# Kernel tuning notes

Measured on AMD Instinct MI355X. Metric: run time of the kernel, lower is better.

Reference implementation:

```python
import jax, jax.numpy as jnp
import numpy as np

DIM = 1024
H = 16
HD = DIM // H  # 64
BASE = 10000.0


def _rope_tables(seq_len, d):
    # freqs over half-dim, then TILED (repeat) along last axis as in the torch code
    freqs = 1.0 / (BASE ** (jnp.arange(0, d, 2, dtype=jnp.float32) / d))  # [d/2]
    t = jnp.arange(seq_len, dtype=jnp.float32)
    f = jnp.outer(t, freqs)  # [S, d/2]
    cos = jnp.concatenate([jnp.cos(f), jnp.cos(f)], axis=-1)  # [S, d] (tiled, NOT interleaved)
    sin = jnp.concatenate([jnp.sin(f), jnp.sin(f)], axis=-1)
    return cos, sin


def _apply_rope(x):
    # x: [B, H, S, d]; rotation pairs adjacent elements (2i, 2i+1)
    S, d = x.shape[-2], x.shape[-1]
    cos, sin = _rope_tables(S, d)  # [S, d]
    xh = x.reshape(*x.shape[:-1], d // 2, 2)
    x_rot = jnp.stack([-xh[..., 1], xh[..., 0]], axis=-1).reshape(x.shape)
    return x * cos + x_rot * sin


def setup_inputs() -> dict:
    key = jax.random.key(0)
    ks = jax.random.split(key, 7)
    B, Sq, Sk = 16, 512, 512
    s = 0.02
    return {
        "x": jax.random.normal(ks[0], (B, Sq, DIM), jnp.float32),
        "context": jax.random.normal(ks[1], (B, Sk, DIM), jnp.float32),
        "Wq": jax.random.normal(ks[2], (DIM, DIM), jnp.float32) * s,
        "Wk": jax.random.normal(ks[3], (DIM, DIM), jnp.float32) * s,
        "Wv": jax.random.normal(ks[4], (DIM, DIM), jnp.float32) * s,
        "Wo": jax.random.normal(ks[5], (DIM, DIM), jnp.float32) * s,
        "bo": jax.random.normal(ks[6], (DIM,), jnp.float32) * s,
    }


def reference(x, context, Wq, Wk, Wv, Wo, bo):
    B, Sq, _ = x.shape
    Sk = context.shape[1]
    scale = HD ** -0.5
    # projections, split heads: [B, H, S, HD]
    q = (x @ Wq).reshape(B, Sq, H, HD).transpose(0, 2, 1, 3)
    k = (context @ Wk).reshape(B, Sk, H, HD).transpose(0, 2, 1, 3)
    v = (context @ Wv).reshape(B, Sk, H, HD).transpose(0, 2, 1, 3)
    q = _apply_rope(q)
    k = _apply_rope(k)
    attn = jax.nn.softmax(jnp.einsum("bhqd,bhkd->bhqk", q, k) * scale, axis=-1)
    out = jnp.einsum("bhqk,bhkd->bhqd", attn, v)
    out = out.transpose(0, 2, 1, 3).reshape(B, Sq, DIM)
    return out @ Wo + bo  # dropout is identity (p=0 / eval)
```

## Files before the change

### kernel.cpp

```cpp
#include <hip/hip_runtime.h>

#define DIM   1024
#define NH    16
#define HD    64
#define BATCH 16
#define SEQ   512
#define MROWS (BATCH*SEQ)
#define SL2E  0.18033688011112042f

typedef __bf16 bf16x8 __attribute__((ext_vector_type(8)));
typedef float  floatx4 __attribute__((ext_vector_type(4)));
typedef short  short4v __attribute__((ext_vector_type(4)));

static __device__ __forceinline__ unsigned short f2bf(float f) {
    union { float f; unsigned u; } v; v.f = f;
    return (unsigned short)((v.u + 0x8000u) >> 16);
}
static __device__ __forceinline__ unsigned pk2(float a, float b) {
    union { float f; unsigned u; } x, y; x.f = a; y.f = b;
    return ((x.u + 0x8000u) >> 16) | ((y.u + 0x8000u) & 0xffff0000u);
}

static __device__ __forceinline__ void glds16(const void* g, void* l) {
    __builtin_amdgcn_global_load_lds(
        (const __attribute__((address_space(1))) unsigned int*)g,
        (__attribute__((address_space(3))) unsigned int*)l, 16, 0, 0);
}

__global__ __launch_bounds__(256)
void prep(const float* __restrict__ x, const float* __restrict__ ctx,
          const float* __restrict__ Wq, const float* __restrict__ Wk,
          const float* __restrict__ Wv, const float* __restrict__ Wo,
          unsigned short* __restrict__ xb, unsigned short* __restrict__ cb,
          unsigned short* __restrict__ WqT, unsigned short* __restrict__ WkT,
          unsigned short* __restrict__ WvT, unsigned short* __restrict__ WoT,
          float2* __restrict__ cstab)
{
    __shared__ float tile[32][33];
    const int blk = blockIdx.x, t = threadIdx.x;
    if (blk < 8192) {
        const float* src = (blk < 4096) ? x : ctx;
        unsigned short* dst = (blk < 4096) ? xb : cb;
        int e = ((blk & 4095) * 256 + t) * 8;
        float4 f0 = *(const float4*)&src[e];
        float4 f1 = *(const float4*)&src[e + 4];
        uint4 o = { pk2(f0.x, f0.y), pk2(f0.z, f0.w), pk2(f1.x, f1.y), pk2(f1.z, f1.w) };
        *(uint4*)&dst[e] = o;
    } else if (blk < 12288) {
        int id2 = blk - 8192;
        const float* W; unsigned short* T;
        switch (id2 >> 10) {
            case 0:  W = Wq; T = WqT; break;
            case 1:  W = Wk; T = WkT; break;
            case 2:  W = Wv; T = WvT; break;
            default: W = Wo; T = WoT; break;
        }
        int local = id2 & 1023;
        int n0 = (local & 31) * 32, k0 = (local >> 5) * 32;
        int tx = t & 31, ty = t >> 5;
        #pragma unroll
        for (int a = 0; a < 4; a++)
            tile[ty + 8 * a][tx] = W[(size_t)(k0 + ty + 8 * a) * DIM + n0 + tx];
        __syncthreads();
        #pragma unroll
        for (int a = 0; a < 4; a++)
            T[(size_t)(n0 + ty + 8 * a) * DIM + k0 + tx] = f2bf(tile[tx][ty + 8 * a]);
    } else {
        int gid = (blk - 12288) * 256 + t;
        int d = gid & (HD - 1), s = gid >> 6;
        const float C = -0.41524101186092f;
        float f = exp2f((float)(d & 31) * C);
        float a = (float)s * f;
        cstab[gid] = make_float2(cosf(a), sinf(a));
    }
}

static __device__ __forceinline__ void gemm_main(
    const unsigned short* __restrict__ A, const unsigned short* __restrict__ Bt,
    int m0, int n0, unsigned short* As, unsigned short* Bs, floatx4 acc[4][4])
{
    const int t = threadIdx.x;
    const int w = t >> 6, l = t & 63;
    const int wm = w >> 1, wn = w & 1;
    const int lane16 = l & 15, quad = l >> 4;
    const int lr = l >> 3;
    const int gsw = ((l & 7) ^ lr) * 8;
    const int co0 = (quad ^ (lane16 & 7)) * 8;
    const int co1 = co0 ^ 32;

    #pragma unroll
    for (int mi = 0; mi < 4; mi++)
        #pragma unroll
        for (int ni = 0; ni < 4; ni++) acc[mi][ni] = (floatx4){0.f, 0.f, 0.f, 0.f};

    const unsigned short* ap = A  + (size_t)(m0 + w * 32 + lr) * DIM + gsw;
    const unsigned short* bp = Bt + (size_t)(n0 + w * 32 + lr) * DIM + gsw;

    for (int kt = 0; kt < DIM; kt += 64) {
        #pragma unroll
        for (int j = 0; j < 4; j++) {
            glds16(ap + (size_t)j * 8 * DIM + kt, &As[(w * 4 + j) * 512]);
            glds16(bp + (size_t)j * 8 * DIM + kt, &Bs[(w * 4 + j) * 512]);
        }
        __syncthreads();
        #pragma unroll
        for (int kk = 0; kk < 2; kk++) {
            const int co = kk ? co1 : co0;
            bf16x8 af[4], bfr[4];
            #pragma unroll
            for (int mi = 0; mi < 4; mi++)
                af[mi] = *(const bf16x8*)&As[(wm * 64 + mi * 16 + lane16) * 64 + co];
            #pragma unroll
            for (int ni = 0; ni < 4; ni++)
                bfr[ni] = *(const bf16x8*)&Bs[(wn * 64 + ni * 16 + lane16) * 64 + co];
            #pragma unroll
            for (int mi = 0; mi < 4; mi++)
                #pragma unroll
                for (int ni = 0; ni < 4; ni++)
                    acc[mi][ni] = __builtin_amdgcn_mfma_f32_16x16x32_bf16(bfr[ni], af[mi], acc[mi][ni], 0, 0, 0);
        }
        __syncthreads();
    }
}

static __device__ __forceinline__ void proj_epilogue(
    unsigned short* __restrict__ Out, const float2* __restrict__ cstab,
    int m0, int n0, int mode, floatx4 acc[4][4])
{
    const int t = threadIdx.x;
    const int w = t >> 6, l = t & 63;
    const int wm = w >> 1, wn = w & 1;
    const int lane16 = l & 15, quad = l >> 4;

    if (mode == 0) {
        #pragma unroll
        for (int mi = 0; mi < 4; mi++) {
            int m = m0 + wm * 64 + mi * 16 + lane16;
            int s = m & 511, b = m >> 9;
            #pragma unroll
            for (int ni = 0; ni < 4; ni++) {
                int n = n0 + wn * 64 + ni * 16 + quad * 4;
                int h = n >> 6, d0 = n & 63;
                const float4* cp = (const float4*)&cstab[s * HD + d0];
                float4 c01 = cp[0];
                float4 c23 = cp[1];
                floatx4 v = acc[mi][ni];
                float r0 = v[0] * c01.x - v[1] * c01.y;
                float r1 = fmaf(v[0], c01.w, v[1] * c01.z);
                float r2 = v[2] * c23.x - v[3] * c23.y;
                float r3 = fmaf(v[2], c23.w, v[3] * c23.z);
                uint2 o = { pk2(r0, r1), pk2(r2, r3) };
                *(uint2*)&Out[((size_t)(b * NH + h) * SEQ + s) * HD + d0] = o;
            }
        }
    } else {
        #pragma unroll
        for (int mi = 0; mi < 4; mi++) {
            int m = m0 + wm * 64 + mi * 16 + lane16;
            #pragma unroll
            for (int ni = 0; ni < 4; ni++) {
                int n = n0 + wn * 64 + ni * 16 + quad * 4;
                floatx4 v = acc[mi][ni];
                uint2 o = { pk2(v[0], v[1]), pk2(v[2], v[3]) };
                *(uint2*)&Out[((size_t)(n >> 9) * DIM + m) * SEQ + (n & 511)] = o;
            }
        }
    }
}

__global__ __launch_bounds__(256)
void proj_qkv(const unsigned short* __restrict__ xb, const unsigned short* __restrict__ cb,
              const unsigned short* __restrict__ WqT, const unsigned short* __restrict__ WkT,
              const unsigned short* __restrict__ WvT,
              unsigned short* __restrict__ Qb, unsigned short* __restrict__ Kb,
              unsigned short* __restrict__ Vtb, const float2* __restrict__ cstab)
{
    __shared__ unsigned short As[128 * 64];
    __shared__ unsigned short Bs[128 * 64];
    const int id = blockIdx.x;
    const int seg = id >> 9, local = id & 511;
    const int xcd = local & 7, seq = local >> 3;
    const unsigned short *A, *Bt; unsigned short* Out;
    int m0, n0, mode;
    if (seg == 0)      { A = cb;  Bt = WkT; Out = Kb;  mode = 0;
                         n0 = (seq & 7) * 128; m0 = (xcd + 8 * (seq >> 3)) * 128; }
    else if (seg == 1) { A = WvT; Bt = cb;  Out = Vtb; mode = 1;
                         m0 = (seq & 7) * 128; n0 = (xcd + 8 * (seq >> 3)) * 128; }
    else               { A = xb;  Bt = WqT; Out = Qb;  mode = 0;
                         n0 = (seq & 7) * 128; m0 = (xcd + 8 * (seq >> 3)) * 128; }
    floatx4 acc[4][4];
    gemm_main(A, Bt, m0, n0, As, Bs, acc);
    proj_epilogue(Out, cstab, m0, n0, mode, acc);
}

__global__ __launch_bounds__(256)
void out_gemm(const unsigned short* __restrict__ Ab, const unsigned short* __restrict__ WoT,
              float* __restrict__ O, const float* __restrict__ bias)
{
    __shared__ unsigned short As[128 * 64];
    __shared__ unsigned short Bs[128 * 64];
    const int id = blockIdx.x;
    const int xcd = id & 7, seq = id >> 3;
    const int n0 = (seq & 7) * 128, m0 = (xcd + 8 * (seq >> 3)) * 128;
    floatx4 acc[4][4];
    gemm_main(Ab, WoT, m0, n0, As, Bs, acc);

    const int t = threadIdx.x;
    const int w = t >> 6, l = t & 63;
    const int wm = w >> 1, wn = w & 1;
    const int lane16 = l & 15, quad = l >> 4;
    #pragma unroll
    for (int ni = 0; ni < 4; ni++) {
        int n = n0 + wn * 64 + ni * 16 + quad * 4;
        float4 bv = *(const float4*)&bias[n];
        #pragma unroll
        for (int mi = 0; mi < 4; mi++) {
            int m = m0 + wm * 64 + mi * 16 + lane16;
            floatx4 v = acc[mi][ni];
            float4 o = { v[0] + bv.x, v[1] + bv.y, v[2] + bv.z, v[3] + bv.w };
            *(float4*)&O[(size_t)m * DIM + n] = o;
        }
    }
}

__global__ __launch_bounds__(256, 4)
void attn_v4(const unsigned short* __restrict__ Q, const unsigned short* __restrict__ K,
             const unsigned short* __restrict__ Vt, unsigned short* __restrict__ Out)
{
    __shared__ unsigned short Qs[128][72];
    __shared__ unsigned short Ks[64][72];
    __shared__ unsigned short Vts[64][72];

    const int id = blockIdx.x;
    const int qi = (id >> 3) & 3;
    const int bh = (id & 7) | ((id >> 5) << 3);
    const int q0 = qi * 128;
    const int t  = threadIdx.x;
    const int w = t >> 6, l = t & 63;
    const int lane16 = l & 15, quad = l >> 4;
    const size_t base = (size_t)bh * SEQ * HD;

    const int sr = t >> 3, sc = (t & 7) * 8;
    #pragma unroll
    for (int j = 0; j < 4; j++)
        *(uint4*)&Qs[j * 32 + sr][sc] =
            *(const uint4*)&Q[base + (size_t)(q0 + j * 32 + sr) * HD + sc];

    const unsigned short* kp0 = K  + base + (size_t)sr * HD + sc;
    const unsigned short* kp1 = kp0 + (size_t)32 * HD;
    const unsigned short* vp0 = Vt + base + (size_t)sr * SEQ + sc;
    const unsigned short* vp1 = vp0 + (size_t)32 * SEQ;

    floatx4 acc_o[2][4];
    float lsum[2] = {0.f, 0.f};
    #pragma unroll
    for (int st = 0; st < 2; st++)
        #pragma unroll
        for (int dt = 0; dt < 4; dt++) acc_o[st][dt] = (floatx4){0.f, 0.f, 0.f, 0.f};

    for (int kt = 0; kt < SEQ; kt += 64) {
        __syncthreads();
        *(uint4*)&Ks[sr][sc]       = *(const uint4*)kp0;  kp0 += 64 * HD;
        *(uint4*)&Ks[sr + 32][sc]  = *(const uint4*)kp1;  kp1 += 64 * HD;
        *(uint4*)&Vts[sr][sc]      = *(const uint4*)vp0;  vp0 += 64;
        *(uint4*)&Vts[sr + 32][sc] = *(const uint4*)vp1;  vp1 += 64;
        __syncthreads();

        bf16x8 kf[2][4];
        #pragma unroll
        for (int kk = 0; kk < 2; kk++)
            #pragma unroll
            for (int c = 0; c < 4; c++)
                kf[kk][c] = *(const bf16x8*)&Ks[c * 16 + lane16][kk * 32 + quad * 8];

        short4v pa[2][4];
        #pragma unroll
        for (int st = 0; st < 2; st++) {
            floatx4 sacc[4];
            #pragma unroll
            for (int c = 0; c < 4; c++) sacc[c] = (floatx4){0.f, 0.f, 0.f, 0.f};
            #pragma unroll
            for (int kk = 0; kk < 2; kk++) {
                bf16x8 qf = *(const bf16x8*)&Qs[st * 64 + w * 16 + lane16][kk * 32 + quad * 8];
                #pragma unroll
                for (int c = 0; c < 4; c++)
                    sacc[c] = __builtin_amdgcn_mfma_f32_16x16x32_bf16(kf[kk][c], qf, sacc[c], 0, 0, 0);
            }
            #pragma unroll
            for (int c = 0; c < 4; c++) {
                short4v pk;
                #pragma unroll
                for (int i = 0; i < 4; i++) {
                    float pv = exp2f(sacc[c][i] * SL2E);
                    lsum[st] += pv;
                    pk[i] = (short)f2bf(pv);
                }
                pa[st][c] = pk;
            }
        }
        #pragma unroll
        for (int c = 0; c < 4; c++) {
            #pragma unroll
            for (int dt = 0; dt < 4; dt++) {
                short4v vf = *(const short4v*)&Vts[dt * 16 + lane16][c * 16 + quad * 4];
                #pragma unroll
                for (int st = 0; st < 2; st++)
                    acc_o[st][dt] = __builtin_amdgcn_mfma_f32_16x16x16bf16_1k(
                        vf, pa[st][c], acc_o[st][dt], 0, 0, 0);
            }
        }
    }

    const int b = bh >> 4, h = bh & 15;
    #pragma unroll
    for (int st = 0; st < 2; st++) {
        float rs = lsum[st];
        rs += __shfl_xor(rs, 16, 64);
        rs += __shfl_xor(rs, 32, 64);
        float inv = 1.0f / rs;
        int s = q0 + st * 64 + w * 16 + lane16;
        size_t rowbase = (size_t)(b * SEQ + s) * DIM + h * HD;
        #pragma unroll
        for (int dt = 0; dt < 4; dt++) {
            floatx4 v = acc_o[st][dt];
            uint2 o = { pk2(v[0] * inv, v[1] * inv), pk2(v[2] * inv, v[3] * inv) };
            *(uint2*)&Out[rowbase + dt * 16 + quad * 4] = o;
        }
    }
}

extern "C" void kernel_launch(void* const* d_in, const int* in_sizes, int n_in,
                              void* d_out, int out_size, void* d_ws, size_t ws_size,
                              hipStream_t stream)
{
    const float* x   = (const float*)d_in[0];
    const float* ctx = (const float*)d_in[1];
    const float* Wq  = (const float*)d_in[2];
    const float* Wk  = (const float*)d_in[3];
    const float* Wv  = (const float*)d_in[4];
    const float* Wo  = (const float*)d_in[5];
    const float* bo  = (const float*)d_in[6];

    const size_t NW = (size_t)DIM * DIM;
    const size_t NB = (size_t)MROWS * DIM;

    unsigned short* x_bf   = (unsigned short*)d_ws;
    unsigned short* ctx_bf = x_bf + NB;
    unsigned short* WqT    = ctx_bf + NB;
    unsigned short* WkT    = WqT + NW;
    unsigned short* WvT    = WkT + NW;
    unsigned short* WoT    = WvT + NW;
    unsigned short* Kb     = WoT + NW;
    unsigned short* Vtb    = Kb + NB;
    float2*         cstab  = (float2*)(Vtb + NB);
    unsigned short* Qb     = (unsigned short*)d_out;
    unsigned short* Ab     = x_bf;

    prep<<<12416, 256, 0, stream>>>(x, ctx, Wq, Wk, Wv, Wo,
                                    x_bf, ctx_bf, WqT, WkT, WvT, WoT, cstab);

    proj_qkv<<<1536, 256, 0, stream>>>(x_bf, ctx_bf, WqT, WkT, WvT,
                                       Qb, Kb, Vtb, cstab);

    attn_v4<<<1024, 256, 0, stream>>>(Qb, Kb, Vtb, Ab);

    out_gemm<<<512, 256, 0, stream>>>(Ab, WoT, (float*)d_out, bo);
}
```

Before: 265.3 us.

## Use double-buffered 128x256 GEMM tiles with 8 waves for projections and output

Replaces the 128x128 single-buffered GEMM main loop with a 128x256 tile computed by 512 threads (2x4 waves). The loop double-buffers LDS, issuing the next k-tile's global-to-LDS loads while MFMAs run on the current tile, with explicit vmcnt waits, barriers and setprio hints. Block-to-tile mapping and grid sizes change to match. The goal is to hide global load latency and get more reuse of each A tile. In exchange it doubles LDS use per block and fewer blocks are launched, which may reduce occupancy.

```diff
diff --git a/kernel.cpp b/kernel.cpp
--- a/kernel.cpp
+++ b/kernel.cpp
@@ -75,13 +75,13 @@
     }
 }
 
-static __device__ __forceinline__ void gemm_main(
+static __device__ __forceinline__ void gemm128x256(
     const unsigned short* __restrict__ A, const unsigned short* __restrict__ Bt,
     int m0, int n0, unsigned short* As, unsigned short* Bs, floatx4 acc[4][4])
 {
     const int t = threadIdx.x;
     const int w = t >> 6, l = t & 63;
-    const int wm = w >> 1, wn = w & 1;
+    const int wm = w >> 2, wn = w & 3;
     const int lane16 = l & 15, quad = l >> 4;
     const int lr = l >> 3;
     const int gsw = ((l & 7) ^ lr) * 8;
@@ -93,34 +93,79 @@
         #pragma unroll
         for (int ni = 0; ni < 4; ni++) acc[mi][ni] = (floatx4){0.f, 0.f, 0.f, 0.f};
 
-    const unsigned short* ap = A  + (size_t)(m0 + w * 32 + lr) * DIM + gsw;
+    const unsigned short* ap = A  + (size_t)(m0 + w * 16 + lr) * DIM + gsw;
     const unsigned short* bp = Bt + (size_t)(n0 + w * 32 + lr) * DIM + gsw;
 
-    for (int kt = 0; kt < DIM; kt += 64) {
-        #pragma unroll
-        for (int j = 0; j < 4; j++) {
-            glds16(ap + (size_t)j * 8 * DIM + kt, &As[(w * 4 + j) * 512]);
-            glds16(bp + (size_t)j * 8 * DIM + kt, &Bs[(w * 4 + j) * 512]);
-        }
-        __syncthreads();
-        #pragma unroll
-        for (int kk = 0; kk < 2; kk++) {
-            const int co = kk ? co1 : co0;
-            bf16x8 af[4], bfr[4];
-            #pragma unroll
-            for (int mi = 0; mi < 4; mi++)
-                af[mi] = *(const bf16x8*)&As[(wm * 64 + mi * 16 + lane16) * 64 + co];
-            #pragma unroll
-            for (int ni = 0; ni < 4; ni++)
-                bfr[ni] = *(const bf16x8*)&Bs[(wn * 64 + ni * 16 + lane16) * 64 + co];
-            #pragma unroll
-            for (int mi = 0; mi < 4; mi++)
-                #pragma unroll
-                for (int ni = 0; ni < 4; ni++)
-                    acc[mi][ni] = __builtin_amdgcn_mfma_f32_16x16x32_bf16(bfr[ni], af[mi], acc[mi][ni], 0, 0, 0);
-        }
-        __syncthreads();
-    }
+    unsigned short* A0 = As;            unsigned short* A1 = As + 8192;
+    unsigned short* B0 = Bs;            unsigned short* B1 = Bs + 16384;
+
+    glds16(ap,                A0 + (w * 2 + 0) * 512);
+    glds16(ap + 8 * DIM,      A0 + (w * 2 + 1) * 512);
+    glds16(bp,                B0 + (w * 4 + 0) * 512);
+    glds16(bp + 8 * DIM,      B0 + (w * 4 + 1) * 512);
+    glds16(bp + 16 * DIM,     B0 + (w * 4 + 2) * 512);
+    glds16(bp + 24 * DIM,     B0 + (w * 4 + 3) * 512);
+
+    int ktn = 64;
+    #pragma unroll 1
+    for (int tt = 0; tt < 16; ++tt) {
+        glds16(ap + ktn,            A1 + (w * 2 + 0) * 512);
+        glds16(ap + 8 * DIM + ktn,  A1 + (w * 2 + 1) * 512);
+        glds16(bp + ktn,            B1 + (w * 4 + 0) * 512);
+        glds16(bp + 8 * DIM + ktn,  B1 + (w * 4 + 1) * 512);
+        asm volatile("s_waitcnt vmcnt(6)" ::: "memory");
+        __builtin_amdgcn_s_barrier();
+        bf16x8 af[4][2], be[2][2];
+        #pragma unroll
+        for (int mi = 0; mi < 4; mi++) {
+            const unsigned short* r = A0 + (wm * 64 + mi * 16 + lane16) * 64;
+            af[mi][0] = *(const bf16x8*)&r[co0];
+            af[mi][1] = *(const bf16x8*)&r[co1];
+        }
+        #pragma unroll
+        for (int e = 0; e < 2; e++) {
+            const unsigned short* r = B0 + (wn * 64 + e * 32 + lane16) * 64;
+            be[e][0] = *(const bf16x8*)&r[co0];
+            be[e][1] = *(const bf16x8*)&r[co1];
+        }
+        asm volatile("s_waitcnt lgkmcnt(0)" ::: "memory");
+        __builtin_amdgcn_sched_barrier(0);
+        __builtin_amdgcn_s_setprio(1);
+        #pragma unroll
+        for (int mi = 0; mi < 4; mi++) {
+            acc[mi][0] = __builtin_amdgcn_mfma_f32_16x16x32_bf16(be[0][0], af[mi][0], acc[mi][0], 0, 0, 0);
+            acc[mi][0] = __builtin_amdgcn_mfma_f32_16x16x32_bf16(be[0][1], af[mi][1], acc[mi][0], 0, 0, 0);
+            acc[mi][2] = __builtin_amdgcn_mfma_f32_16x16x32_bf16(be[1][0], af[mi][0], acc[mi][2], 0, 0, 0);
+            acc[mi][2] = __builtin_amdgcn_mfma_f32_16x16x32_bf16(be[1][1], af[mi][1], acc[mi][2], 0, 0, 0);
+        }
+        __builtin_amdgcn_s_setprio(0);
+        glds16(bp + 16 * DIM + ktn, B1 + (w * 4 + 2) * 512);
+        glds16(bp + 24 * DIM + ktn, B1 + (w * 4 + 3) * 512);
+        asm volatile("s_waitcnt vmcnt(6)" ::: "memory");
+        __builtin_amdgcn_s_barrier();
+        bf16x8 bo_[2][2];
+        #pragma unroll
+        for (int e = 0; e < 2; e++) {
+            const unsigned short* r = B0 + (wn * 64 + e * 32 + 16 + lane16) * 64;
+            bo_[e][0] = *(const bf16x8*)&r[co0];
+            bo_[e][1] = *(const bf16x8*)&r[co1];
+        }
+        asm volatile("s_waitcnt lgkmcnt(0)" ::: "memory");
+        __builtin_amdgcn_sched_barrier(0);
+        __builtin_amdgcn_s_setprio(1);
+        #pragma unroll
+        for (int mi = 0; mi < 4; mi++) {
+            acc[mi][1] = __builtin_amdgcn_mfma_f32_16x16x32_bf16(bo_[0][0], af[mi][0], acc[mi][1], 0, 0, 0);
+            acc[mi][1] = __builtin_amdgcn_mfma_f32_16x16x32_bf16(bo_[0][1], af[mi][1], acc[mi][1], 0, 0, 0);
+            acc[mi][3] = __builtin_amdgcn_mfma_f32_16x16x32_bf16(bo_[1][0], af[mi][0], acc[mi][3], 0, 0, 0);
+            acc[mi][3] = __builtin_amdgcn_mfma_f32_16x16x32_bf16(bo_[1][1], af[mi][1], acc[mi][3], 0, 0, 0);
+        }
+        __builtin_amdgcn_s_setprio(0);
+        unsigned short* ta = A0; A0 = A1; A1 = ta;
+        unsigned short* tb = B0; B0 = B1; B1 = tb;
+        ktn = (ktn + 64) & (DIM - 1);
+    }
+    asm volatile("s_waitcnt vmcnt(0)" ::: "memory");
 }
 
 static __device__ __forceinline__ void proj_epilogue(
@@ -129,7 +174,7 @@
 {
     const int t = threadIdx.x;
     const int w = t >> 6, l = t & 63;
-    const int wm = w >> 1, wn = w & 1;
+    const int wm = w >> 2, wn = w & 3;
     const int lane16 = l & 15, quad = l >> 4;
 
     if (mode == 0) {
@@ -168,46 +213,48 @@
     }
 }
 
-__global__ __launch_bounds__(256)
+__global__ __launch_bounds__(512, 2)
 void proj_qkv(const unsigned short* __restrict__ xb, const unsigned short* __restrict__ cb,
               const unsigned short* __restrict__ WqT, const unsigned short* __restrict__ WkT,
               const unsigned short* __restrict__ WvT,
               unsigned short* __restrict__ Qb, unsigned short* __restrict__ Kb,
               unsigned short* __restrict__ Vtb, const float2* __restrict__ cstab)
 {
-    __shared__ unsigned short As[128 * 64];
-    __shared__ unsigned short Bs[128 * 64];
+    __shared__ unsigned short As[2 * 128 * 64];
+    __shared__ unsigned short Bs[2 * 256 * 64];
     const int id = blockIdx.x;
-    const int seg = id >> 9, local = id & 511;
-    const int xcd = local & 7, seq = local >> 3;
+    const int seg = id >> 8, local = id & 255;
     const unsigned short *A, *Bt; unsigned short* Out;
     int m0, n0, mode;
     if (seg == 0)      { A = cb;  Bt = WkT; Out = Kb;  mode = 0;
-                         n0 = (seq & 7) * 128; m0 = (xcd + 8 * (seq >> 3)) * 128; }
+                         m0 = ((local & 7) + 8 * (local >> 5)) * 128;
+                         n0 = ((local >> 3) & 3) * 256; }
     else if (seg == 1) { A = WvT; Bt = cb;  Out = Vtb; mode = 1;
-                         m0 = (seq & 7) * 128; n0 = (xcd + 8 * (seq >> 3)) * 128; }
+                         m0 = ((local >> 3) & 7) * 128;
+                         n0 = ((local & 7) + 8 * (local >> 6)) * 256; }
     else               { A = xb;  Bt = WqT; Out = Qb;  mode = 0;
-                         n0 = (seq & 7) * 128; m0 = (xcd + 8 * (seq >> 3)) * 128; }
+                         m0 = ((local & 7) + 8 * (local >> 5)) * 128;
+                         n0 = ((local >> 3) & 3) * 256; }
     floatx4 acc[4][4];
-    gemm_main(A, Bt, m0, n0, As, Bs, acc);
+    gemm128x256(A, Bt, m0, n0, As, Bs, acc);
     proj_epilogue(Out, cstab, m0, n0, mode, acc);
 }
 
-__global__ __launch_bounds__(256)
+__global__ __launch_bounds__(512, 2)
 void out_gemm(const unsigned short* __restrict__ Ab, const unsigned short* __restrict__ WoT,
               float* __restrict__ O, const float* __restrict__ bias)
 {
-    __shared__ unsigned short As[128 * 64];
-    __shared__ unsigned short Bs[128 * 64];
+    __shared__ unsigned short As[2 * 128 * 64];
+    __shared__ unsigned short Bs[2 * 256 * 64];
     const int id = blockIdx.x;
-    const int xcd = id & 7, seq = id >> 3;
-    const int n0 = (seq & 7) * 128, m0 = (xcd + 8 * (seq >> 3)) * 128;
+    const int m0 = ((id & 7) + 8 * (id >> 5)) * 128;
+    const int n0 = ((id >> 3) & 3) * 256;
     floatx4 acc[4][4];
-    gemm_main(Ab, WoT, m0, n0, As, Bs, acc);
+    gemm128x256(Ab, WoT, m0, n0, As, Bs, acc);
 
     const int t = threadIdx.x;
     const int w = t >> 6, l = t & 63;
-    const int wm = w >> 1, wn = w & 1;
+    const int wm = w >> 2, wn = w & 3;
     const int lane16 = l & 15, quad = l >> 4;
     #pragma unroll
     for (int ni = 0; ni < 4; ni++) {
@@ -359,10 +406,10 @@
     prep<<<12416, 256, 0, stream>>>(x, ctx, Wq, Wk, Wv, Wo,
                                     x_bf, ctx_bf, WqT, WkT, WvT, WoT, cstab);
 
-    proj_qkv<<<1536, 256, 0, stream>>>(x_bf, ctx_bf, WqT, WkT, WvT,
-                                       Qb, Kb, Vtb, cstab);
+    proj_qkv<<<768, 512, 0, stream>>>(x_bf, ctx_bf, WqT, WkT, WvT,
+                                      Qb, Kb, Vtb, cstab);
 
     attn_v4<<<1024, 256, 0, stream>>>(Qb, Kb, Vtb, Ab);
 
-    out_gemm<<<512, 256, 0, stream>>>(Ab, WoT, (float*)d_out, bo);
-}
+    out_gemm<<<256, 512, 0, stream>>>(Ab, WoT, (float*)d_out, bo);
+}
```

After: 261.5 us. About the same (-1.4%).

## Rewrite projection GEMMs as 256x256 tiles with double-buffered LDS pipeline

Applied to the files above, without the earlier changes.

Replaces the 128x128 single-buffered GEMM core with a 256x256 tile using 8 waves, double-buffered LDS, and staged async global-to-LDS loads interleaved with MFMA quarters under barriers and priority raising. Grid sizes for the QKV projection and output GEMM shrink accordingly, with a new block-to-tile mapping. The aim is to raise arithmetic intensity and overlap memory loads with matrix-core work. The cost is that 128 KB of LDS per block limits occupancy, and the 128-block output GEMM may underfill the GPU.

```diff
diff --git a/kernel.cpp b/kernel.cpp
--- a/kernel.cpp
+++ b/kernel.cpp
@@ -75,13 +75,46 @@
     }
 }
 
-static __device__ __forceinline__ void gemm_main(
+template<int AH>
+static __device__ __forceinline__ void rdA(const unsigned short* Ab, int wm, int lane16,
+                                           int co0, int co1, bf16x8 af[4][2]) {
+    #pragma unroll
+    for (int mi = 0; mi < 4; mi++) {
+        const unsigned short* r = Ab + (wm * 128 + AH * 64 + mi * 16 + lane16) * 64;
+        af[mi][0] = *(const bf16x8*)&r[co0];
+        af[mi][1] = *(const bf16x8*)&r[co1];
+    }
+}
+template<int BH>
+static __device__ __forceinline__ void rdB(const unsigned short* Bb, int wn, int lane16,
+                                           int co0, int co1, bf16x8 bfv[2][2]) {
+    #pragma unroll
+    for (int ni = 0; ni < 2; ni++) {
+        const unsigned short* r = Bb + (wn * 64 + BH * 32 + ni * 16 + lane16) * 64;
+        bfv[ni][0] = *(const bf16x8*)&r[co0];
+        bfv[ni][1] = *(const bf16x8*)&r[co1];
+    }
+}
+template<int AH, int BH>
+static __device__ __forceinline__ void mmq(bf16x8 bfv[2][2], bf16x8 af[4][2], floatx4 acc[8][4]) {
+    #pragma unroll
+    for (int mi = 0; mi < 4; mi++)
+        #pragma unroll
+        for (int ni = 0; ni < 2; ni++) {
+            floatx4 c = acc[AH * 4 + mi][BH * 2 + ni];
+            c = __builtin_amdgcn_mfma_f32_16x16x32_bf16(bfv[ni][0], af[mi][0], c, 0, 0, 0);
+            c = __builtin_amdgcn_mfma_f32_16x16x32_bf16(bfv[ni][1], af[mi][1], c, 0, 0, 0);
+            acc[AH * 4 + mi][BH * 2 + ni] = c;
+        }
+}
+
+static __device__ __forceinline__ void gemm256(
     const unsigned short* __restrict__ A, const unsigned short* __restrict__ Bt,
-    int m0, int n0, unsigned short* As, unsigned short* Bs, floatx4 acc[4][4])
+    int m0, int n0, unsigned short* As, unsigned short* Bs, floatx4 acc[8][4])
 {
     const int t = threadIdx.x;
     const int w = t >> 6, l = t & 63;
-    const int wm = w >> 1, wn = w & 1;
+    const int wm = w >> 2, wn = w & 3;
     const int lane16 = l & 15, quad = l >> 4;
     const int lr = l >> 3;
     const int gsw = ((l & 7) ^ lr) * 8;
@@ -89,53 +122,120 @@
     const int co1 = co0 ^ 32;
 
     #pragma unroll
-    for (int mi = 0; mi < 4; mi++)
-        #pragma unroll
-        for (int ni = 0; ni < 4; ni++) acc[mi][ni] = (floatx4){0.f, 0.f, 0.f, 0.f};
-
-    const unsigned short* ap = A  + (size_t)(m0 + w * 32 + lr) * DIM + gsw;
-    const unsigned short* bp = Bt + (size_t)(n0 + w * 32 + lr) * DIM + gsw;
-
-    for (int kt = 0; kt < DIM; kt += 64) {
-        #pragma unroll
-        for (int j = 0; j < 4; j++) {
-            glds16(ap + (size_t)j * 8 * DIM + kt, &As[(w * 4 + j) * 512]);
-            glds16(bp + (size_t)j * 8 * DIM + kt, &Bs[(w * 4 + j) * 512]);
-        }
-        __syncthreads();
-        #pragma unroll
-        for (int kk = 0; kk < 2; kk++) {
-            const int co = kk ? co1 : co0;
-            bf16x8 af[4], bfr[4];
-            #pragma unroll
-            for (int mi = 0; mi < 4; mi++)
-                af[mi] = *(const bf16x8*)&As[(wm * 64 + mi * 16 + lane16) * 64 + co];
-            #pragma unroll
-            for (int ni = 0; ni < 4; ni++)
-                bfr[ni] = *(const bf16x8*)&Bs[(wn * 64 + ni * 16 + lane16) * 64 + co];
-            #pragma unroll
-            for (int mi = 0; mi < 4; mi++)
-                #pragma unroll
-                for (int ni = 0; ni < 4; ni++)
-                    acc[mi][ni] = __builtin_amdgcn_mfma_f32_16x16x32_bf16(bfr[ni], af[mi], acc[mi][ni], 0, 0, 0);
-        }
-        __syncthreads();
-    }
+    for (int i = 0; i < 8; i++)
+        #pragma unroll
+        for (int j = 0; j < 4; j++) acc[i][j] = (floatx4){0.f, 0.f, 0.f, 0.f};
+
+    const unsigned short *aU0[2], *bU1[2];
+    int dU0[2], dU1[2];
+    #pragma unroll
+    for (int j = 0; j < 2; j++) {
+        int uj = w * 16 + j * 8 + lr;
+        int ub = w * 16 + j * 8;
+        int rA0  = uj + (uj & 64);
+        int rA0b = ub + (ub & 64);
+        aU0[j] = A + (size_t)(m0 + rA0) * DIM + gsw;
+        dU0[j] = rA0b * 64;
+        int rB1  = ((uj >> 5) << 6) + (uj & 31);
+        int rB1b = ((ub >> 5) << 6) + (ub & 31);
+        bU1[j] = Bt + (size_t)(n0 + rB1) * DIM + gsw;
+        dU1[j] = rB1b * 64;
+    }
+    unsigned short* Ae = As;            unsigned short* Ao = As + 16384;
+    unsigned short* Be = Bs;            unsigned short* Bo = Bs + 16384;
+
+#define STG_U0(buf, kt) { glds16(aU0[0] + (kt), (buf) + dU0[0]); \
+                          glds16(aU0[1] + (kt), (buf) + dU0[1]); }
+#define STG_U3(buf, kt) { glds16(aU0[0] + (size_t)64 * DIM + (kt), (buf) + dU0[0] + 4096); \
+                          glds16(aU0[1] + (size_t)64 * DIM + (kt), (buf) + dU0[1] + 4096); }
+#define STG_U1(buf, kt) { glds16(bU1[0] + (kt), (buf) + dU1[0]); \
+                          glds16(bU1[1] + (kt), (buf) + dU1[1]); }
+#define STG_U2(buf, kt) { glds16(bU1[0] + (size_t)32 * DIM + (kt), (buf) + dU1[0] + 2048); \
+                          glds16(bU1[1] + (size_t)32 * DIM + (kt), (buf) + dU1[1] + 2048); }
+#define BAR_MFMA(MM) \
+    __builtin_amdgcn_s_barrier(); \
+    asm volatile("s_waitcnt lgkmcnt(0)" ::: "memory"); \
+    __builtin_amdgcn_sched_barrier(0); \
+    __builtin_amdgcn_s_setprio(1); \
+    MM; \
+    __builtin_amdgcn_s_setprio(0); \
+    __builtin_amdgcn_s_barrier();
+
+    STG_U0(Ae, 0); STG_U1(Be, 0); STG_U2(Be, 0); STG_U3(Ae, 0);
+    STG_U0(Ao, 64); STG_U1(Bo, 64); STG_U2(Bo, 64);
+    asm volatile("s_waitcnt vmcnt(6)" ::: "memory");
+    __builtin_amdgcn_s_barrier();
+
+    bf16x8 af[4][2], b0[2][2], b1[2][2];
+
+    #pragma unroll 1
+    for (int i = 0; i < 7; i++) {
+        const int k1 = (2 * i + 1) * 64, k2 = k1 + 64, k3 = k2 + 64;
+        STG_U3(Ao, k1);
+        rdA<0>(Ae, wm, lane16, co0, co1, af);
+        rdB<0>(Be, wn, lane16, co0, co1, b0);
+        BAR_MFMA((mmq<0, 0>(b0, af, acc)));
+        STG_U0(Ae, k2);
+        rdB<1>(Be, wn, lane16, co0, co1, b1);
+        BAR_MFMA((mmq<0, 1>(b1, af, acc)));
+        STG_U1(Be, k2);
+        rdA<1>(Ae, wm, lane16, co0, co1, af);
+        BAR_MFMA((mmq<1, 0>(b0, af, acc)));
+        STG_U2(Be, k2);
+        asm volatile("s_waitcnt vmcnt(6)" ::: "memory");
+        BAR_MFMA((mmq<1, 1>(b1, af, acc)));
+        STG_U3(Ae, k2);
+        rdA<0>(Ao, wm, lane16, co0, co1, af);
+        rdB<0>(Bo, wn, lane16, co0, co1, b0);
+        BAR_MFMA((mmq<0, 0>(b0, af, acc)));
+        STG_U0(Ao, k3);
+        rdB<1>(Bo, wn, lane16, co0, co1, b1);
+        BAR_MFMA((mmq<0, 1>(b1, af, acc)));
+        STG_U1(Bo, k3);
+        rdA<1>(Ao, wm, lane16, co0, co1, af);
+        BAR_MFMA((mmq<1, 0>(b0, af, acc)));
+        STG_U2(Bo, k3);
+        asm volatile("s_waitcnt vmcnt(6)" ::: "memory");
+        BAR_MFMA((mmq<1, 1>(b1, af, acc)));
+    }
+    STG_U3(Ao, 15 * 64);
+    rdA<0>(Ae, wm, lane16, co0, co1, af);
+    rdB<0>(Be, wn, lane16, co0, co1, b0);
+    BAR_MFMA((mmq<0, 0>(b0, af, acc)));
+    rdB<1>(Be, wn, lane16, co0, co1, b1);
+    BAR_MFMA((mmq<0, 1>(b1, af, acc)));
+    rdA<1>(Ae, wm, lane16, co0, co1, af);
+    BAR_MFMA((mmq<1, 0>(b0, af, acc)));
+    asm volatile("s_waitcnt vmcnt(0)" ::: "memory");
+    BAR_MFMA((mmq<1, 1>(b1, af, acc)));
+    rdA<0>(Ao, wm, lane16, co0, co1, af);
+    rdB<0>(Bo, wn, lane16, co0, co1, b0);
+    BAR_MFMA((mmq<0, 0>(b0, af, acc)));
+    rdB<1>(Bo, wn, lane16, co0, co1, b1);
+    BAR_MFMA((mmq<0, 1>(b1, af, acc)));
+    rdA<1>(Ao, wm, lane16, co0, co1, af);
+    BAR_MFMA((mmq<1, 0>(b0, af, acc)));
+    BAR_MFMA((mmq<1, 1>(b1, af, acc)));
+#undef STG_U0
+#undef STG_U1
+#undef STG_U2
+#undef STG_U3
+#undef BAR_MFMA
 }
 
 static __device__ __forceinline__ void proj_epilogue(
     unsigned short* __restrict__ Out, const float2* __restrict__ cstab,
-    int m0, int n0, int mode, floatx4 acc[4][4])
+    int m0, int n0, int mode, floatx4 acc[8][4])
 {
     const int t = threadIdx.x;
     const int w = t >> 6, l = t & 63;
-    const int wm = w >> 1, wn = w & 1;
+    const int wm = w >> 2, wn = w & 3;
     const int lane16 = l & 15, quad = l >> 4;
 
     if (mode == 0) {
         #pragma unroll
-        for (int mi = 0; mi < 4; mi++) {
-            int m = m0 + wm * 64 + mi * 16 + lane16;
+        for (int mi = 0; mi < 8; mi++) {
+            int m = m0 + wm * 128 + mi * 16 + lane16;
             int s = m & 511, b = m >> 9;
             #pragma unroll
             for (int ni = 0; ni < 4; ni++) {
@@ -155,8 +255,8 @@
         }
     } else {
         #pragma unroll
-        for (int mi = 0; mi < 4; mi++) {
-            int m = m0 + wm * 64 + mi * 16 + lane16;
+        for (int mi = 0; mi < 8; mi++) {
+            int m = m0 + wm * 128 + mi * 16 + lane16;
             #pragma unroll
             for (int ni = 0; ni < 4; ni++) {
                 int n = n0 + wn * 64 + ni * 16 + quad * 4;
@@ -168,54 +268,55 @@
     }
 }
 
-__global__ __launch_bounds__(256)
+__global__ __launch_bounds__(512, 2)
 void proj_qkv(const unsigned short* __restrict__ xb, const unsigned short* __restrict__ cb,
               const unsigned short* __restrict__ WqT, const unsigned short* __restrict__ WkT,
               const unsigned short* __restrict__ WvT,
               unsigned short* __restrict__ Qb, unsigned short* __restrict__ Kb,
               unsigned short* __restrict__ Vtb, const float2* __restrict__ cstab)
 {
-    __shared__ unsigned short As[128 * 64];
-    __shared__ unsigned short Bs[128 * 64];
+    __shared__ unsigned short As[2 * 256 * 64];
+    __shared__ unsigned short Bs[2 * 256 * 64];
     const int id = blockIdx.x;
-    const int seg = id >> 9, local = id & 511;
-    const int xcd = local & 7, seq = local >> 3;
+    const int seg = id >> 7, local = id & 127;
+    const int big = (local & 7) + (local >> 5) * 8;
+    const int sml = (local >> 3) & 3;
     const unsigned short *A, *Bt; unsigned short* Out;
     int m0, n0, mode;
     if (seg == 0)      { A = cb;  Bt = WkT; Out = Kb;  mode = 0;
-                         n0 = (seq & 7) * 128; m0 = (xcd + 8 * (seq >> 3)) * 128; }
+                         m0 = big * 256; n0 = sml * 256; }
     else if (seg == 1) { A = WvT; Bt = cb;  Out = Vtb; mode = 1;
-                         m0 = (seq & 7) * 128; n0 = (xcd + 8 * (seq >> 3)) * 128; }
+                         m0 = sml * 256; n0 = big * 256; }
     else               { A = xb;  Bt = WqT; Out = Qb;  mode = 0;
-                         n0 = (seq & 7) * 128; m0 = (xcd + 8 * (seq >> 3)) * 128; }
-    floatx4 acc[4][4];
-    gemm_main(A, Bt, m0, n0, As, Bs, acc);
+                         m0 = big * 256; n0 = sml * 256; }
+    floatx4 acc[8][4];
+    gemm256(A, Bt, m0, n0, As, Bs, acc);
     proj_epilogue(Out, cstab, m0, n0, mode, acc);
 }
 
-__global__ __launch_bounds__(256)
+__global__ __launch_bounds__(512, 2)
 void out_gemm(const unsigned short* __restrict__ Ab, const unsigned short* __restrict__ WoT,
               float* __restrict__ O, const float* __restrict__ bias)
 {
-    __shared__ unsigned short As[128 * 64];
-    __shared__ unsigned short Bs[128 * 64];
+    __shared__ unsigned short As[2 * 256 * 64];
+    __shared__ unsigned short Bs[2 * 256 * 64];
     const int id = blockIdx.x;
-    const int xcd = id & 7, seq = id >> 3;
-    const int n0 = (seq & 7) * 128, m0 = (xcd + 8 * (seq >> 3)) * 128;
-    floatx4 acc[4][4];
-    gemm_main(Ab, WoT, m0, n0, As, Bs, acc);
+    const int m0 = ((id & 7) + (id >> 5) * 8) * 256;
+    const int n0 = ((id >> 3) & 3) * 256;
+    floatx4 acc[8][4];
+    gemm256(Ab, WoT, m0, n0, As, Bs, acc);
 
     const int t = threadIdx.x;
     const int w = t >> 6, l = t & 63;
-    const int wm = w >> 1, wn = w & 1;
+    const int wm = w >> 2, wn = w & 3;
     const int lane16 = l & 15, quad = l >> 4;
     #pragma unroll
     for (int ni = 0; ni < 4; ni++) {
         int n = n0 + wn * 64 + ni * 16 + quad * 4;
         float4 bv = *(const float4*)&bias[n];
         #pragma unroll
-        for (int mi = 0; mi < 4; mi++) {
-            int m = m0 + wm * 64 + mi * 16 + lane16;
+        for (int mi = 0; mi < 8; mi++) {
+            int m = m0 + wm * 128 + mi * 16 + lane16;
             floatx4 v = acc[mi][ni];
             float4 o = { v[0] + bv.x, v[1] + bv.y, v[2] + bv.z, v[3] + bv.w };
             *(float4*)&O[(size_t)m * DIM + n] = o;
@@ -359,10 +460,10 @@
     prep<<<12416, 256, 0, stream>>>(x, ctx, Wq, Wk, Wv, Wo,
                                     x_bf, ctx_bf, WqT, WkT, WvT, WoT, cstab);
 
-    proj_qkv<<<1536, 256, 0, stream>>>(x_bf, ctx_bf, WqT, WkT, WvT,
-                                       Qb, Kb, Vtb, cstab);
+    proj_qkv<<<384, 512, 0, stream>>>(x_bf, ctx_bf, WqT, WkT, WvT,
+                                      Qb, Kb, Vtb, cstab);
 
     attn_v4<<<1024, 256, 0, stream>>>(Qb, Kb, Vtb, Ab);
 
-    out_gemm<<<512, 256, 0, stream>>>(Ab, WoT, (float*)d_out, bo);
-}
+    out_gemm<<<128, 512, 0, stream>>>(Ab, WoT, (float*)d_out, bo);
+}
```

Result: slower. 299.5 us (+12.9%).
